# Optimization experiments

Hardware: AMD Instinct MI355X
Metric: run time of the kernel (lower is better)

Reference implementation:

```python
import jax, jax.numpy as jnp
import numpy as np

E = 1024
H = 16
D = E // H  # projection_dim = 64


def setup_inputs() -> dict:
    key = jax.random.key(0)
    ks = jax.random.split(key, 9)
    s = 1.0 / np.sqrt(E)
    return {
        "inputs": jax.random.normal(ks[0], (2, 2048, E), dtype=jnp.float32),
        "Wq": jax.random.uniform(ks[1], (E, E), jnp.float32, -s, s),
        "bq": jax.random.uniform(ks[2], (E,), jnp.float32, -s, s),
        "Wk": jax.random.uniform(ks[3], (E, E), jnp.float32, -s, s),
        "bk": jax.random.uniform(ks[4], (E,), jnp.float32, -s, s),
        "Wv": jax.random.uniform(ks[5], (E, E), jnp.float32, -s, s),
        "bv": jax.random.uniform(ks[6], (E,), jnp.float32, -s, s),
        "Wo": jax.random.uniform(ks[7], (E, E), jnp.float32, -s, s),
        "bo": jax.random.uniform(ks[8], (E,), jnp.float32, -s, s),
    }


def reference(inputs, Wq, bq, Wk, bk, Wv, bv, Wo, bo):
    B, S, _ = inputs.shape
    # Linear layers use y = x @ W.T + b (torch convention); weights here stored as [E,E]
    q = inputs @ Wq.T + bq
    k = inputs @ Wk.T + bk
    v = inputs @ Wv.T + bv
    # separate heads: [B,S,E] -> [B,H,S,D]
    q = q.reshape(B, S, H, D).transpose(0, 2, 1, 3)
    k = k.reshape(B, S, H, D).transpose(0, 2, 1, 3)
    v = v.reshape(B, S, H, D).transpose(0, 2, 1, 3)
    scale = 1.0 / jnp.sqrt(jnp.float32(D))
    scores = jnp.einsum('bhqd,bhkd->bhqk', q, k) * scale  # [B,H,S,S]
    weights = jax.nn.softmax(scores, axis=-1)
    attn = jnp.einsum('bhqk,bhkd->bhqd', weights, v)  # [B,H,S,D]
    concat = attn.transpose(0, 2, 1, 3).reshape(B, S, E)
    # dropout is identity in eval mode
    return concat @ Wo.T + bo
```

## Files before the change

kernel.cpp:

```cpp
#include <hip/hip_runtime.h>
#include <hip/hip_bf16.h>
#include <stdint.h>

#define E_ 1024
#define H_ 16
#define D_ 64
#define B_ 2
#define S_ 2048
#define M_ 4096

typedef __bf16 bf16_t;
typedef __bf16 bf16x8 __attribute__((ext_vector_type(8)));
typedef __bf16 bf16x4 __attribute__((ext_vector_type(4)));
typedef __bf16 bf16x2 __attribute__((ext_vector_type(2)));
typedef float  f32x4  __attribute__((ext_vector_type(4)));
typedef float  f32x16 __attribute__((ext_vector_type(16)));
typedef unsigned int u32x2 __attribute__((ext_vector_type(2)));
typedef unsigned int u32x4 __attribute__((ext_vector_type(4)));

__global__ __launch_bounds__(256) void cvt_f32_to_bf16(const float* __restrict__ src,
                                                       bf16_t* __restrict__ dst, int n4) {
  int i = blockIdx.x * blockDim.x + threadIdx.x;
  if (i < n4) {
    float4 v = reinterpret_cast<const float4*>(src)[i];
    bf16x4 o;
    o[0] = (bf16_t)v.x; o[1] = (bf16_t)v.y; o[2] = (bf16_t)v.z; o[3] = (bf16_t)v.w;
    reinterpret_cast<bf16x4*>(dst)[i] = o;
  }
}

__global__ __launch_bounds__(256) void cvt_weights(
    const float* __restrict__ w0, const float* __restrict__ w1,
    const float* __restrict__ w2, const float* __restrict__ w3,
    bf16_t* __restrict__ d0, bf16_t* __restrict__ d1,
    bf16_t* __restrict__ d2, bf16_t* __restrict__ d3) {
  const int z = blockIdx.y;
  const float* src = (z == 0) ? w0 : (z == 1) ? w1 : (z == 2) ? w2 : w3;
  bf16_t* dst = (z == 0) ? d0 : (z == 1) ? d1 : (z == 2) ? d2 : d3;
  int i = blockIdx.x * blockDim.x + threadIdx.x;
  float4 v = reinterpret_cast<const float4*>(src)[i];
  bf16x4 o;
  o[0] = (bf16_t)v.x; o[1] = (bf16_t)v.y; o[2] = (bf16_t)v.z; o[3] = (bf16_t)v.w;
  reinterpret_cast<bf16x4*>(dst)[i] = o;
}

static __device__ __forceinline__ void gl_lds16(const bf16_t* g, bf16_t* l) {
  __builtin_amdgcn_global_load_lds((__attribute__((address_space(1))) void*)g,
                                   (__attribute__((address_space(3))) void*)l,
                                   16, 0, 0);
}

static __device__ __forceinline__ void gemm128_mainloop(
    const bf16_t* __restrict__ Ag, const bf16_t* __restrict__ Bg,
    bf16_t* ldsA, bf16_t* ldsB, int m0, int n0, f32x4 acc[4][4]) {
  const int tid  = threadIdx.x;
  const int lane = tid & 63, wave = tid >> 6;
  const int lrow = lane & 15, lgrp = lane >> 4;
  const int wr = (wave >> 1) * 64, wc = (wave & 1) * 64;
  const int skol = (lane & 3) * 8;
  const f32x4 zero = {0.f, 0.f, 0.f, 0.f};
#pragma unroll
  for (int i = 0; i < 4; i++)
#pragma unroll
    for (int j = 0; j < 4; j++) acc[i][j] = zero;

#pragma unroll
  for (int t = 0; t < 2; t++) {
    int c = wave * 2 + t;
    int row = c * 16 + (lane >> 2);
    gl_lds16(Ag + (size_t)(m0 + row) * E_ + skol, ldsA + c * 512);
    gl_lds16(Bg + (size_t)(n0 + row) * E_ + skol, ldsB + c * 512);
  }

  for (int kt = 0; kt < E_ / 32; ++kt) {
    __syncthreads();
    bf16x8 fA[4], fB[4];
#pragma unroll
    for (int i = 0; i < 4; i++)
      fA[i] = *reinterpret_cast<const bf16x8*>(ldsA + (wr + i * 16 + lrow) * 32 + lgrp * 8);
#pragma unroll
    for (int j = 0; j < 4; j++)
      fB[j] = *reinterpret_cast<const bf16x8*>(ldsB + (wc + j * 16 + lrow) * 32 + lgrp * 8);
    __builtin_amdgcn_s_setprio(1);
#pragma unroll
    for (int i = 0; i < 4; i++)
#pragma unroll
      for (int j = 0; j < 4; j++)
        acc[i][j] = __builtin_amdgcn_mfma_f32_16x16x32_bf16(fA[i], fB[j], acc[i][j], 0, 0, 0);
    __builtin_amdgcn_s_setprio(0);
    if (kt + 1 < E_ / 32) {
      __syncthreads();
      const int k0 = (kt + 1) * 32;
#pragma unroll
      for (int t = 0; t < 2; t++) {
        int c = wave * 2 + t;
        int row = c * 16 + (lane >> 2);
        gl_lds16(Ag + (size_t)(m0 + row) * E_ + k0 + skol, ldsA + c * 512);
        gl_lds16(Bg + (size_t)(n0 + row) * E_ + k0 + skol, ldsB + c * 512);
      }
    }
  }
}

__global__ __launch_bounds__(256) void qkv_gemm(
    const bf16_t* __restrict__ xbf,
    const bf16_t* __restrict__ Wqb, const bf16_t* __restrict__ Wkb, const bf16_t* __restrict__ Wvb,
    const float* __restrict__ bq, const float* __restrict__ bk, const float* __restrict__ bv,
    bf16_t* __restrict__ Qo, bf16_t* __restrict__ Ko, bf16_t* __restrict__ Vt) {
  __shared__ alignas(16) bf16_t ldsA[128 * 32];
  __shared__ alignas(16) bf16_t ldsB[128 * 32];
  const int z = blockIdx.z;
  const bf16_t* W   = (z == 0) ? Wqb : ((z == 1) ? Wkb : Wvb);
  const float* bias = (z == 0) ? bq  : ((z == 1) ? bk  : bv);
  const int m0 = blockIdx.x * 128, n0 = blockIdx.y * 128;
  f32x4 acc[4][4];
  gemm128_mainloop(xbf, W, ldsA, ldsB, m0, n0, acc);

  const int lane = threadIdx.x & 63, wave = threadIdx.x >> 6;
  const int lrow = lane & 15, lgrp = lane >> 4;
  const int wr = (wave >> 1) * 64, wc = (wave & 1) * 64;
  const float scale = (z == 0) ? 0.18033688011112042f : 1.0f;
#pragma unroll
  for (int i = 0; i < 4; i++) {
    const int mbase = m0 + wr + i * 16 + lgrp * 4;
    const int b = mbase >> 11, s = mbase & (S_ - 1);
#pragma unroll
    for (int j = 0; j < 4; j++) {
      const int n = n0 + wc + j * 16 + lrow;
      const float bn = bias[n];
      const int h = n >> 6, d = n & 63;
      if (z == 2) {
        bf16x4 v;
#pragma unroll
        for (int r = 0; r < 4; r++) v[r] = (bf16_t)(acc[i][j][r] + bn);
        *reinterpret_cast<bf16x4*>(Vt + ((size_t)((b * H_ + h) * D_ + d)) * S_ + s) = v;
      } else {
        bf16_t* O = (z == 0) ? Qo : Ko;
#pragma unroll
        for (int r = 0; r < 4; r++)
          O[((size_t)((b * H_ + h) * S_) + (s + r)) * D_ + d] = (bf16_t)((acc[i][j][r] + bn) * scale);
      }
    }
  }
}

__global__ __launch_bounds__(256) void out_gemm(
    const bf16_t* __restrict__ Cbf, const bf16_t* __restrict__ Wob,
    const float* __restrict__ bo, float* __restrict__ out) {
  __shared__ alignas(16) bf16_t ldsA[128 * 32];
  __shared__ alignas(16) bf16_t ldsB[128 * 32];
  const int m0 = blockIdx.x * 128, n0 = blockIdx.y * 128;
  f32x4 acc[4][4];
  gemm128_mainloop(Cbf, Wob, ldsA, ldsB, m0, n0, acc);

  const int lane = threadIdx.x & 63, wave = threadIdx.x >> 6;
  const int lrow = lane & 15, lgrp = lane >> 4;
  const int wr = (wave >> 1) * 64, wc = (wave & 1) * 64;
#pragma unroll
  for (int i = 0; i < 4; i++) {
    const int mbase = m0 + wr + i * 16 + lgrp * 4;
#pragma unroll
    for (int j = 0; j < 4; j++) {
      const int n = n0 + wc + j * 16 + lrow;
      const float bn = bo[n];
#pragma unroll
      for (int r = 0; r < 4; r++)
        out[(size_t)(mbase + r) * E_ + n] = acc[i][j][r] + bn;
    }
  }
}


static __device__ __forceinline__ unsigned pack2(float a, float b) {
  bf16x2 t; t[0] = (bf16_t)a; t[1] = (bf16_t)b;
  return __builtin_bit_cast(unsigned, t);
}

static __device__ __forceinline__ bf16x8 mkfrag(unsigned a0, unsigned a1,
                                                unsigned a2, unsigned a3) {
  u32x2 s02 = __builtin_amdgcn_permlane32_swap(a0, a2, false, false);
  u32x2 s13 = __builtin_amdgcn_permlane32_swap(a1, a3, false, false);
  u32x4 t; t[0] = s02[0]; t[1] = s13[0]; t[2] = s02[1]; t[3] = s13[1];
  return *reinterpret_cast<bf16x8*>(&t);
}

__global__ __launch_bounds__(512) void attn_kernel(
    const bf16_t* __restrict__ Qg, const bf16_t* __restrict__ Kg,
    const bf16_t* __restrict__ Vtg, bf16_t* __restrict__ Og) {
  __shared__ alignas(16) bf16_t Kl[2][2][64 * 64];
  __shared__ alignas(16) bf16_t Vl[2][2][64 * 64];
  const int bh = blockIdx.y;
  const int q0 = blockIdx.x * 128;
  const int tid = threadIdx.x, lane = tid & 63, wave = tid >> 6;
  const int qsub = wave & 3, kvg = wave >> 2;
  const int ql = lane & 31, hi = lane >> 5;
  const bf16_t* Qb = Qg + (size_t)bh * S_ * D_;
  const bf16_t* Kb = Kg + (size_t)bh * S_ * D_;
  const bf16_t* Vb = Vtg + (size_t)bh * D_ * S_;

  const int q = q0 + qsub * 32 + ql;
  bf16x8 qf[4];
#pragma unroll
  for (int ds = 0; ds < 4; ds++)
    qf[ds] = *reinterpret_cast<const bf16x8*>(Qb + (size_t)q * D_ + ds * 16 + hi * 8);

  f32x16 o0, o1;
#pragma unroll
  for (int r = 0; r < 16; r++) { o0[r] = 0.f; o1[r] = 0.f; }
  float li = 0.f;

  const int srow_lo = lane >> 3;
  const int sunit = lane & 7;

#pragma unroll
  for (int p = 0; p < 2; p++) {
    int c = p * 4 + qsub;
    int row = c * 8 + srow_lo;
    int u = sunit ^ (row & 7);
    gl_lds16(Kb + (size_t)(kvg * 64 + row) * D_ + u * 8, &Kl[kvg][0][c * 512]);
    gl_lds16(Vb + (size_t)row * S_ + kvg * 64 + u * 8, &Vl[kvg][0][c * 512]);
  }
  __syncthreads();

  for (int it = 0; it < S_ / 128; ++it) {
    const int cur = it & 1;
    if (it + 1 < S_ / 128) {
      const int kvn = (kvg + (it + 1) * 2) * 64;
#pragma unroll
      for (int p = 0; p < 2; p++) {
        int c = p * 4 + qsub;
        int row = c * 8 + srow_lo;
        int u = sunit ^ (row & 7);
        gl_lds16(Kb + (size_t)(kvn + row) * D_ + u * 8, &Kl[kvg][cur ^ 1][c * 512]);
        gl_lds16(Vb + (size_t)row * S_ + kvn + u * 8, &Vl[kvg][cur ^ 1][c * 512]);
      }
    }
    const char* kbuf = reinterpret_cast<const char*>(&Kl[kvg][cur][0]);
    const char* vbuf = reinterpret_cast<const char*>(&Vl[kvg][cur][0]);

    f32x16 pa0, pa1;
#pragma unroll
    for (int r = 0; r < 16; r++) { pa0[r] = 0.f; pa1[r] = 0.f; }
    __builtin_amdgcn_s_setprio(1);
#pragma unroll
    for (int ds = 0; ds < 4; ds++) {
      {
        const int krow = ql;
        const int u = (ds * 2 + hi) ^ (krow & 7);
        bf16x8 kf = *reinterpret_cast<const bf16x8*>(kbuf + krow * 128 + u * 16);
        pa0 = __builtin_amdgcn_mfma_f32_32x32x16_bf16(kf, qf[ds], pa0, 0, 0, 0);
      }
      {
        const int krow = 32 + ql;
        const int u = (ds * 2 + hi) ^ (krow & 7);
        bf16x8 kf = *reinterpret_cast<const bf16x8*>(kbuf + krow * 128 + u * 16);
        pa1 = __builtin_amdgcn_mfma_f32_32x32x16_bf16(kf, qf[ds], pa1, 0, 0, 0);
      }
    }
    __builtin_amdgcn_s_setprio(0);

    float ps = 0.f;
#pragma unroll
    for (int r = 0; r < 16; r++) {
      pa0[r] = __builtin_amdgcn_exp2f(pa0[r]); ps += pa0[r];
      pa1[r] = __builtin_amdgcn_exp2f(pa1[r]); ps += pa1[r];
    }
    {
      u32x2 ss = __builtin_amdgcn_permlane32_swap(
          __builtin_bit_cast(unsigned, ps), __builtin_bit_cast(unsigned, ps), false, false);
      ps = __builtin_bit_cast(float, ss[0]) + __builtin_bit_cast(float, ss[1]);
    }
    li += ps;

    unsigned w0[8], w1[8];
#pragma unroll
    for (int i = 0; i < 8; i++) {
      w0[i] = pack2(pa0[2 * i], pa0[2 * i + 1]);
      w1[i] = pack2(pa1[2 * i], pa1[2 * i + 1]);
    }
    bf16x8 bfr[4];
    bfr[0] = mkfrag(w0[0], w0[1], w0[2], w0[3]);
    bfr[1] = mkfrag(w0[4], w0[5], w0[6], w0[7]);
    bfr[2] = mkfrag(w1[0], w1[1], w1[2], w1[3]);
    bfr[3] = mkfrag(w1[4], w1[5], w1[6], w1[7]);

    __builtin_amdgcn_s_setprio(1);
#pragma unroll
    for (int step = 0; step < 4; step++) {
      {
        const int vrow = ql;
        const int u = (step * 2 + hi) ^ (vrow & 7);
        bf16x8 vf = *reinterpret_cast<const bf16x8*>(vbuf + vrow * 128 + u * 16);
        o0 = __builtin_amdgcn_mfma_f32_32x32x16_bf16(vf, bfr[step], o0, 0, 0, 0);
      }
      {
        const int vrow = 32 + ql;
        const int u = (step * 2 + hi) ^ (vrow & 7);
        bf16x8 vf = *reinterpret_cast<const bf16x8*>(vbuf + vrow * 128 + u * 16);
        o1 = __builtin_amdgcn_mfma_f32_32x32x16_bf16(vf, bfr[step], o1, 0, 0, 0);
      }
    }
    __builtin_amdgcn_s_setprio(0);

    __syncthreads();
  }

  f32x4* smO = reinterpret_cast<f32x4*>(&Kl[0][0][0]);
  float* smL = reinterpret_cast<float*>(&Vl[0][0][0]);
  const int mi_ = qsub * 64 + lane;
  if (kvg == 1) {
#pragma unroll
    for (int g = 0; g < 4; g++) {
      f32x4 a;
#pragma unroll
      for (int i = 0; i < 4; i++) a[i] = o0[g * 4 + i];
      smO[g * 256 + mi_] = a;
    }
#pragma unroll
    for (int g = 0; g < 4; g++) {
      f32x4 a;
#pragma unroll
      for (int i = 0; i < 4; i++) a[i] = o1[g * 4 + i];
      smO[(g + 4) * 256 + mi_] = a;
    }
    smL[mi_] = li;
  }
  __syncthreads();
  if (kvg == 0) {
    li += smL[mi_];
#pragma unroll
    for (int g = 0; g < 4; g++) {
      f32x4 a = smO[g * 256 + mi_];
#pragma unroll
      for (int i = 0; i < 4; i++) o0[g * 4 + i] += a[i];
    }
#pragma unroll
    for (int g = 0; g < 4; g++) {
      f32x4 a = smO[(g + 4) * 256 + mi_];
#pragma unroll
      for (int i = 0; i < 4; i++) o1[g * 4 + i] += a[i];
    }
    const float inv = 1.0f / li;
    const int b = bh >> 4, h = bh & 15;
    bf16_t* orow = Og + (size_t)(b * S_ + q) * E_ + h * 64;
#pragma unroll
    for (int g = 0; g < 4; g++) {
      bf16x4 v;
#pragma unroll
      for (int i = 0; i < 4; i++) v[i] = (bf16_t)(o0[g * 4 + i] * inv);
      *reinterpret_cast<bf16x4*>(orow + g * 8 + hi * 4) = v;
    }
#pragma unroll
    for (int g = 0; g < 4; g++) {
      bf16x4 v;
#pragma unroll
      for (int i = 0; i < 4; i++) v[i] = (bf16_t)(o1[g * 4 + i] * inv);
      *reinterpret_cast<bf16x4*>(orow + 32 + g * 8 + hi * 4) = v;
    }
  }
}

extern "C" void kernel_launch(void* const* d_in, const int* in_sizes, int n_in,
                              void* d_out, int out_size, void* d_ws, size_t ws_size,
                              hipStream_t stream) {
  (void)in_sizes; (void)n_in; (void)out_size; (void)ws_size;
  const float* x  = (const float*)d_in[0];
  const float* Wq = (const float*)d_in[1];
  const float* bq = (const float*)d_in[2];
  const float* Wk = (const float*)d_in[3];
  const float* bk = (const float*)d_in[4];
  const float* Wv = (const float*)d_in[5];
  const float* bv = (const float*)d_in[6];
  const float* Wo = (const float*)d_in[7];
  const float* bo = (const float*)d_in[8];
  float* out = (float*)d_out;

  bf16_t* ws  = (bf16_t*)d_ws;
  bf16_t* xbf = ws;
  bf16_t* Ct  = ws;
  bf16_t* wqb = ws + (4u << 20);
  bf16_t* wkb = ws + (5u << 20);
  bf16_t* wvb = ws + (6u << 20);
  bf16_t* wob = ws + (7u << 20);
  bf16_t* Qt  = ws + (8u << 20);
  bf16_t* Kt  = ws + (12u << 20);
  bf16_t* Vt  = ws + (16u << 20);

  cvt_f32_to_bf16<<<4096, 256, 0, stream>>>(x, xbf, 1 << 20);
  cvt_weights<<<dim3(1024, 4), 256, 0, stream>>>(Wq, Wk, Wv, Wo, wqb, wkb, wvb, wob);

  qkv_gemm<<<dim3(32, 8, 3), 256, 0, stream>>>(xbf, wqb, wkb, wvb, bq, bk, bv, Qt, Kt, Vt);
  attn_kernel<<<dim3(16, 32), 512, 0, stream>>>(Qt, Kt, Vt, Ct);
  out_gemm<<<dim3(32, 8), 256, 0, stream>>>(Ct, wob, bo, out);
}
```

Measured before the change: 118.3 us.

## Double-buffer GEMM LDS tiles, swap MFMA operands for vector stores, remap attention grid

The shared GEMM mainloop now keeps two LDS buffers, so the next K-tile's global-to-LDS load is issued before the current tile's MFMAs and each iteration needs one barrier instead of two. A template flag swaps the MFMA operands so the accumulator is transposed, which lets the Q/K and output epilogues write contiguous 4-wide vectors and load bias as a float4. The attention launch becomes a flat 1D grid with a custom mapping from block index to (batch-head, q-tile), meant to spread heads across XCDs for better cache locality. The cost is twice the LDS per GEMM block, which may lower occupancy, and the s_setprio hints are dropped.

```diff
diff --git a/kernel.cpp b/kernel.cpp
--- a/kernel.cpp
+++ b/kernel.cpp
@@ -50,55 +50,57 @@
                                    16, 0, 0);
 }
 
+template <int SWAP>
 static __device__ __forceinline__ void gemm128_mainloop(
     const bf16_t* __restrict__ Ag, const bf16_t* __restrict__ Bg,
-    bf16_t* ldsA, bf16_t* ldsB, int m0, int n0, f32x4 acc[4][4]) {
+    bf16_t* ldsA0, bf16_t* ldsA1, bf16_t* ldsB0, bf16_t* ldsB1,
+    int m0, int n0, f32x4 acc[4][4]) {
   const int tid  = threadIdx.x;
   const int lane = tid & 63, wave = tid >> 6;
   const int lrow = lane & 15, lgrp = lane >> 4;
   const int wr = (wave >> 1) * 64, wc = (wave & 1) * 64;
   const int skol = (lane & 3) * 8;
+  const int c0 = wave * 2;
+  const int rowA = c0 * 16 + (lane >> 2);
   const f32x4 zero = {0.f, 0.f, 0.f, 0.f};
 #pragma unroll
   for (int i = 0; i < 4; i++)
 #pragma unroll
     for (int j = 0; j < 4; j++) acc[i][j] = zero;
 
-#pragma unroll
-  for (int t = 0; t < 2; t++) {
-    int c = wave * 2 + t;
-    int row = c * 16 + (lane >> 2);
-    gl_lds16(Ag + (size_t)(m0 + row) * E_ + skol, ldsA + c * 512);
-    gl_lds16(Bg + (size_t)(n0 + row) * E_ + skol, ldsB + c * 512);
-  }
+  gl_lds16(Ag + (size_t)(m0 + rowA) * E_ + skol,      ldsA0 + c0 * 512);
+  gl_lds16(Ag + (size_t)(m0 + rowA + 16) * E_ + skol, ldsA0 + (c0 + 1) * 512);
+  gl_lds16(Bg + (size_t)(n0 + rowA) * E_ + skol,      ldsB0 + c0 * 512);
+  gl_lds16(Bg + (size_t)(n0 + rowA + 16) * E_ + skol, ldsB0 + (c0 + 1) * 512);
+  __syncthreads();
 
   for (int kt = 0; kt < E_ / 32; ++kt) {
+    bf16_t* sA = (kt & 1) ? ldsA1 : ldsA0;
+    bf16_t* sB = (kt & 1) ? ldsB1 : ldsB0;
+    if (kt + 1 < E_ / 32) {
+      bf16_t* dA = (kt & 1) ? ldsA0 : ldsA1;
+      bf16_t* dB = (kt & 1) ? ldsB0 : ldsB1;
+      const int k0 = (kt + 1) * 32;
+      gl_lds16(Ag + (size_t)(m0 + rowA) * E_ + k0 + skol,      dA + c0 * 512);
+      gl_lds16(Ag + (size_t)(m0 + rowA + 16) * E_ + k0 + skol, dA + (c0 + 1) * 512);
+      gl_lds16(Bg + (size_t)(n0 + rowA) * E_ + k0 + skol,      dB + c0 * 512);
+      gl_lds16(Bg + (size_t)(n0 + rowA + 16) * E_ + k0 + skol, dB + (c0 + 1) * 512);
+    }
+    bf16x8 fA[4], fB[4];
+#pragma unroll
+    for (int i = 0; i < 4; i++)
+      fA[i] = *reinterpret_cast<const bf16x8*>(sA + (wr + i * 16 + lrow) * 32 + lgrp * 8);
+#pragma unroll
+    for (int j = 0; j < 4; j++)
+      fB[j] = *reinterpret_cast<const bf16x8*>(sB + (wc + j * 16 + lrow) * 32 + lgrp * 8);
+#pragma unroll
+    for (int i = 0; i < 4; i++)
+#pragma unroll
+      for (int j = 0; j < 4; j++)
+        acc[i][j] = SWAP
+          ? __builtin_amdgcn_mfma_f32_16x16x32_bf16(fB[j], fA[i], acc[i][j], 0, 0, 0)
+          : __builtin_amdgcn_mfma_f32_16x16x32_bf16(fA[i], fB[j], acc[i][j], 0, 0, 0);
     __syncthreads();
-    bf16x8 fA[4], fB[4];
-#pragma unroll
-    for (int i = 0; i < 4; i++)
-      fA[i] = *reinterpret_cast<const bf16x8*>(ldsA + (wr + i * 16 + lrow) * 32 + lgrp * 8);
-#pragma unroll
-    for (int j = 0; j < 4; j++)
-      fB[j] = *reinterpret_cast<const bf16x8*>(ldsB + (wc + j * 16 + lrow) * 32 + lgrp * 8);
-    __builtin_amdgcn_s_setprio(1);
-#pragma unroll
-    for (int i = 0; i < 4; i++)
-#pragma unroll
-      for (int j = 0; j < 4; j++)
-        acc[i][j] = __builtin_amdgcn_mfma_f32_16x16x32_bf16(fA[i], fB[j], acc[i][j], 0, 0, 0);
-    __builtin_amdgcn_s_setprio(0);
-    if (kt + 1 < E_ / 32) {
-      __syncthreads();
-      const int k0 = (kt + 1) * 32;
-#pragma unroll
-      for (int t = 0; t < 2; t++) {
-        int c = wave * 2 + t;
-        int row = c * 16 + (lane >> 2);
-        gl_lds16(Ag + (size_t)(m0 + row) * E_ + k0 + skol, ldsA + c * 512);
-        gl_lds16(Bg + (size_t)(n0 + row) * E_ + k0 + skol, ldsB + c * 512);
-      }
-    }
   }
 }
 
@@ -107,38 +109,51 @@
     const bf16_t* __restrict__ Wqb, const bf16_t* __restrict__ Wkb, const bf16_t* __restrict__ Wvb,
     const float* __restrict__ bq, const float* __restrict__ bk, const float* __restrict__ bv,
     bf16_t* __restrict__ Qo, bf16_t* __restrict__ Ko, bf16_t* __restrict__ Vt) {
-  __shared__ alignas(16) bf16_t ldsA[128 * 32];
-  __shared__ alignas(16) bf16_t ldsB[128 * 32];
+  __shared__ alignas(16) bf16_t ldsA[2][128 * 32];
+  __shared__ alignas(16) bf16_t ldsB[2][128 * 32];
   const int z = blockIdx.z;
   const bf16_t* W   = (z == 0) ? Wqb : ((z == 1) ? Wkb : Wvb);
   const float* bias = (z == 0) ? bq  : ((z == 1) ? bk  : bv);
   const int m0 = blockIdx.x * 128, n0 = blockIdx.y * 128;
-  f32x4 acc[4][4];
-  gemm128_mainloop(xbf, W, ldsA, ldsB, m0, n0, acc);
-
   const int lane = threadIdx.x & 63, wave = threadIdx.x >> 6;
   const int lrow = lane & 15, lgrp = lane >> 4;
   const int wr = (wave >> 1) * 64, wc = (wave & 1) * 64;
-  const float scale = (z == 0) ? 0.18033688011112042f : 1.0f;
-#pragma unroll
-  for (int i = 0; i < 4; i++) {
-    const int mbase = m0 + wr + i * 16 + lgrp * 4;
-    const int b = mbase >> 11, s = mbase & (S_ - 1);
-#pragma unroll
-    for (int j = 0; j < 4; j++) {
-      const int n = n0 + wc + j * 16 + lrow;
-      const float bn = bias[n];
-      const int h = n >> 6, d = n & 63;
-      if (z == 2) {
+  f32x4 acc[4][4];
+
+  if (z == 2) {
+    gemm128_mainloop<0>(xbf, W, ldsA[0], ldsA[1], ldsB[0], ldsB[1], m0, n0, acc);
+#pragma unroll
+    for (int i = 0; i < 4; i++) {
+      const int mbase = m0 + wr + i * 16 + lgrp * 4;
+      const int b = mbase >> 11, s = mbase & (S_ - 1);
+#pragma unroll
+      for (int j = 0; j < 4; j++) {
+        const int n = n0 + wc + j * 16 + lrow;
+        const float bn = bias[n];
+        const int h = n >> 6, d = n & 63;
         bf16x4 v;
 #pragma unroll
         for (int r = 0; r < 4; r++) v[r] = (bf16_t)(acc[i][j][r] + bn);
         *reinterpret_cast<bf16x4*>(Vt + ((size_t)((b * H_ + h) * D_ + d)) * S_ + s) = v;
-      } else {
-        bf16_t* O = (z == 0) ? Qo : Ko;
-#pragma unroll
-        for (int r = 0; r < 4; r++)
-          O[((size_t)((b * H_ + h) * S_) + (s + r)) * D_ + d] = (bf16_t)((acc[i][j][r] + bn) * scale);
+      }
+    }
+  } else {
+    gemm128_mainloop<1>(xbf, W, ldsA[0], ldsA[1], ldsB[0], ldsB[1], m0, n0, acc);
+    bf16_t* O = (z == 0) ? Qo : Ko;
+    const float scale = (z == 0) ? 0.18033688011112042f : 1.0f;
+#pragma unroll
+    for (int i = 0; i < 4; i++) {
+      const int m = m0 + wr + i * 16 + lrow;
+      const int b = m >> 11, s = m & (S_ - 1);
+#pragma unroll
+      for (int j = 0; j < 4; j++) {
+        const int nb = n0 + wc + j * 16 + lgrp * 4;
+        const int h = nb >> 6, d = nb & 63;
+        const f32x4 b4 = *reinterpret_cast<const f32x4*>(bias + nb);
+        bf16x4 v;
+#pragma unroll
+        for (int r = 0; r < 4; r++) v[r] = (bf16_t)((acc[i][j][r] + b4[r]) * scale);
+        *reinterpret_cast<bf16x4*>(O + ((size_t)((b * H_ + h) * S_) + s) * D_ + d) = v;
       }
     }
   }
@@ -147,25 +162,24 @@
 __global__ __launch_bounds__(256) void out_gemm(
     const bf16_t* __restrict__ Cbf, const bf16_t* __restrict__ Wob,
     const float* __restrict__ bo, float* __restrict__ out) {
-  __shared__ alignas(16) bf16_t ldsA[128 * 32];
-  __shared__ alignas(16) bf16_t ldsB[128 * 32];
+  __shared__ alignas(16) bf16_t ldsA[2][128 * 32];
+  __shared__ alignas(16) bf16_t ldsB[2][128 * 32];
   const int m0 = blockIdx.x * 128, n0 = blockIdx.y * 128;
   f32x4 acc[4][4];
-  gemm128_mainloop(Cbf, Wob, ldsA, ldsB, m0, n0, acc);
+  gemm128_mainloop<1>(Cbf, Wob, ldsA[0], ldsA[1], ldsB[0], ldsB[1], m0, n0, acc);
 
   const int lane = threadIdx.x & 63, wave = threadIdx.x >> 6;
   const int lrow = lane & 15, lgrp = lane >> 4;
   const int wr = (wave >> 1) * 64, wc = (wave & 1) * 64;
 #pragma unroll
   for (int i = 0; i < 4; i++) {
-    const int mbase = m0 + wr + i * 16 + lgrp * 4;
+    const int m = m0 + wr + i * 16 + lrow;
 #pragma unroll
     for (int j = 0; j < 4; j++) {
-      const int n = n0 + wc + j * 16 + lrow;
-      const float bn = bo[n];
-#pragma unroll
-      for (int r = 0; r < 4; r++)
-        out[(size_t)(mbase + r) * E_ + n] = acc[i][j][r] + bn;
+      const int nb = n0 + wc + j * 16 + lgrp * 4;
+      const f32x4 b4 = *reinterpret_cast<const f32x4*>(bo + nb);
+      f32x4 v = acc[i][j] + b4;
+      *reinterpret_cast<f32x4*>(out + (size_t)m * E_ + nb) = v;
     }
   }
 }
@@ -189,8 +203,9 @@
     const bf16_t* __restrict__ Vtg, bf16_t* __restrict__ Og) {
   __shared__ alignas(16) bf16_t Kl[2][2][64 * 64];
   __shared__ alignas(16) bf16_t Vl[2][2][64 * 64];
-  const int bh = blockIdx.y;
-  const int q0 = blockIdx.x * 128;
+  const int f = blockIdx.x;
+  const int bh = (f & 7) * 4 + (f >> 7);
+  const int q0 = ((f >> 3) & 15) * 128;
   const int tid = threadIdx.x, lane = tid & 63, wave = tid >> 6;
   const int qsub = wave & 3, kvg = wave >> 2;
   const int ql = lane & 31, hi = lane >> 5;
@@ -390,6 +405,6 @@
   cvt_weights<<<dim3(1024, 4), 256, 0, stream>>>(Wq, Wk, Wv, Wo, wqb, wkb, wvb, wob);
 
   qkv_gemm<<<dim3(32, 8, 3), 256, 0, stream>>>(xbf, wqb, wkb, wvb, bq, bk, bv, Qt, Kt, Vt);
-  attn_kernel<<<dim3(16, 32), 512, 0, stream>>>(Qt, Kt, Vt, Ct);
+  attn_kernel<<<512, 512, 0, stream>>>(Qt, Kt, Vt, Ct);
   out_gemm<<<dim3(32, 8), 256, 0, stream>>>(Ct, wob, bo, out);
 }
```

After: 118.0 us. About the same (-0.3%).
